# Performance work log

Hardware: AMD Instinct MI355X
Metric: run time of the kernel (lower is better)

The kernel has to match this reference:

```python
import jax, jax.numpy as jnp
import numpy as np

VOCAB = 32000
HID = 1024
LAYERS = 2
BATCH = 16
SEQ = 256


def setup_inputs() -> dict:
    key = jax.random.key(0)
    ks = jax.random.split(key, 8)
    s = 1.0 / np.sqrt(HID)
    x = jax.random.randint(ks[0], (BATCH, SEQ), 0, VOCAB, dtype=jnp.int64)
    embed = jax.random.normal(ks[1], (VOCAB, HID), dtype=jnp.float32) * 0.02
    Wi = jax.random.uniform(ks[2], (LAYERS, HID, HID), jnp.float32, -s, s)
    bi = jax.random.uniform(ks[3], (LAYERS, HID), jnp.float32, -s, s)
    Wh = jax.random.uniform(ks[4], (LAYERS, HID, HID), jnp.float32, -s, s)
    bh = jax.random.uniform(ks[5], (LAYERS, HID), jnp.float32, -s, s)
    Wo = jax.random.uniform(ks[6], (VOCAB, HID), jnp.float32, -s, s)
    bo = jax.random.uniform(ks[7], (VOCAB,), jnp.float32, -s, s)
    return {"x": x, "embed": embed, "Wi": Wi, "bi": bi, "Wh": Wh, "bh": bh, "Wo": Wo, "bo": bo}


def reference(x, embed, Wi, bi, Wh, bh, Wo, bo):
    B, S = x.shape
    L, H, _ = Wi.shape
    emb = embed[x]                      # [B, S, H]
    emb_t = jnp.swapaxes(emb, 0, 1)     # [S, B, H]
    h0 = jnp.zeros((L, B, H), dtype=embed.dtype)

    def step(hidden, x_t):
        inp = x_t
        new_h = []
        for l in range(L):
            inp = jnp.tanh(inp @ Wi[l].T + bi[l] + hidden[l] @ Wh[l].T + bh[l])
            new_h.append(inp)
        hidden = jnp.stack(new_h)       # [L, B, H]
        return hidden, inp              # emit top-layer hidden per step

    hidden, tops = jax.lax.scan(step, h0, emb_t)   # tops: [S, B, H]
    # project all steps at once (same math as per-step fc_out)
    logits = jnp.einsum('sbh,vh->bsv', tops, Wo) + bo  # [B, S, V]
    return logits, hidden
```

## Files before the change

### kernel.cpp

```cpp
#include <hip/hip_runtime.h>
#include <cmath>
#include <cstdint>

#define VOCAB 32000
#define HID   1024
#define BATCH 16
#define SEQ   256
#define NL0   64
#define NL1   128
#define MASTER (NL0 + NL1)
#define NBLK  (NL0 + NL1 + 1)
#define BH    (BATCH * HID)

typedef __attribute__((ext_vector_type(8))) short short8;
typedef __attribute__((ext_vector_type(4))) float f32x4;

__device__ __forceinline__ ushort f2bf(float f) {
  uint u = __builtin_bit_cast(uint, f);
  return (ushort)((u + 0x7FFFu + ((u >> 16) & 1u)) >> 16);
}
__device__ __forceinline__ float bf2f(ushort h) {
  return __builtin_bit_cast(float, (uint)h << 16);
}

#define LOAD8(d, base)                                                        \
  asm volatile(                                                               \
    "global_load_dwordx4 %0, %8, off sc0 sc1\n\t"                             \
    "global_load_dwordx4 %1, %8, off offset:512 sc0 sc1\n\t"                  \
    "global_load_dwordx4 %2, %8, off offset:1024 sc0 sc1\n\t"                 \
    "global_load_dwordx4 %3, %8, off offset:1536 sc0 sc1\n\t"                 \
    "global_load_dwordx4 %4, %8, off offset:2048 sc0 sc1\n\t"                 \
    "global_load_dwordx4 %5, %8, off offset:2560 sc0 sc1\n\t"                 \
    "global_load_dwordx4 %6, %8, off offset:3072 sc0 sc1\n\t"                 \
    "global_load_dwordx4 %7, %8, off offset:3584 sc0 sc1"                     \
    : "=&v"(d[0]), "=&v"(d[1]), "=&v"(d[2]), "=&v"(d[3]),                     \
      "=&v"(d[4]), "=&v"(d[5]), "=&v"(d[6]), "=&v"(d[7])                      \
    : "v"(base) : "memory")

#define WAIT8(d)                                                              \
  asm volatile("s_waitcnt vmcnt(0)"                                           \
    : "+v"(d[0]), "+v"(d[1]), "+v"(d[2]), "+v"(d[3]),                         \
      "+v"(d[4]), "+v"(d[5]), "+v"(d[6]), "+v"(d[7]) :: "memory")

__device__ __forceinline__ void st_coherent(float* p, float v) {
  asm volatile("global_store_dword %0, %1, off sc0 sc1" :: "v"(p), "v"(v) : "memory");
}
__device__ __forceinline__ int ld_rlx(const int* p) {
  return __hip_atomic_load(p, __ATOMIC_RELAXED, __HIP_MEMORY_SCOPE_AGENT);
}
__device__ __forceinline__ void st_rlx(int* p, int v) {
  __hip_atomic_store(p, v, __ATOMIC_RELAXED, __HIP_MEMORY_SCOPE_AGENT);
}

__global__ __launch_bounds__(256) void pre0_gemm(
    const int* __restrict__ x, const float* __restrict__ embed,
    const float* __restrict__ Wi0, const float* __restrict__ bi0,
    const float* __restrict__ bh0, float* __restrict__ pre)
{
  __shared__ float As[32][132];
  __shared__ float Bs[32][132];
  const int tid  = threadIdx.x;
  const int n0   = blockIdx.x * 128;
  const int m0   = blockIdx.y * 128;
  const int lrow = tid >> 3, lkq = tid & 7;
  const int ty   = tid >> 4, tx  = tid & 15;

  const float* arow[4];
#pragma unroll
  for (int q = 0; q < 4; ++q) {
    int m = m0 + lrow + 32 * q;
    int t = m >> 4, b = m & 15;
    arow[q] = embed + (size_t)x[b * SEQ + t] * HID;
  }
  const float* brow = Wi0 + (size_t)(n0 + lrow) * HID;

  float acc[8][8];
#pragma unroll
  for (int i = 0; i < 8; ++i)
#pragma unroll
    for (int j = 0; j < 8; ++j) acc[i][j] = 0.f;

  for (int kt = 0; kt < HID; kt += 32) {
    float4 av[4], bv[4];
#pragma unroll
    for (int q = 0; q < 4; ++q) {
      av[q] = *(const float4*)(arow[q] + kt + lkq * 4);
      bv[q] = *(const float4*)(brow + (size_t)(32 * q) * HID + kt + lkq * 4);
    }
    __syncthreads();
#pragma unroll
    for (int q = 0; q < 4; ++q) {
      int r = lrow + 32 * q;
      As[lkq*4+0][r] = av[q].x; As[lkq*4+1][r] = av[q].y;
      As[lkq*4+2][r] = av[q].z; As[lkq*4+3][r] = av[q].w;
      Bs[lkq*4+0][r] = bv[q].x; Bs[lkq*4+1][r] = bv[q].y;
      Bs[lkq*4+2][r] = bv[q].z; Bs[lkq*4+3][r] = bv[q].w;
    }
    __syncthreads();
#pragma unroll
    for (int kk = 0; kk < 32; ++kk) {
      float4 a0 = *(const float4*)&As[kk][ty * 8];
      float4 a1 = *(const float4*)&As[kk][ty * 8 + 4];
      float4 b0 = *(const float4*)&Bs[kk][tx * 8];
      float4 b1 = *(const float4*)&Bs[kk][tx * 8 + 4];
      float a[8] = {a0.x,a0.y,a0.z,a0.w,a1.x,a1.y,a1.z,a1.w};
      float b[8] = {b0.x,b0.y,b0.z,b0.w,b1.x,b1.y,b1.z,b1.w};
#pragma unroll
      for (int i = 0; i < 8; ++i)
#pragma unroll
        for (int j = 0; j < 8; ++j) acc[i][j] = fmaf(a[i], b[j], acc[i][j]);
    }
  }

#pragma unroll
  for (int i = 0; i < 8; ++i) {
    int m = m0 + ty * 8 + i;
    float* o = pre + (size_t)m * HID + n0 + tx * 8;
#pragma unroll
    for (int j = 0; j < 8; ++j) {
      int n = n0 + tx * 8 + j;
      o[j] = acc[i][j] + bi0[n] + bh0[n];
    }
  }
}

__global__ __launch_bounds__(512) void rnn_scan(
    const float* __restrict__ Wi, const float* __restrict__ Wh,
    const float* __restrict__ bi, const float* __restrict__ bh,
    const float* __restrict__ pre0, float* __restrict__ h0ring,
    float* __restrict__ h1g, float* __restrict__ tops,
    int* __restrict__ bar)
{
  const int tid = threadIdx.x;
  const int blk = blockIdx.x;
  int* go0 = bar + 12 * 32;
  int* go1 = bar + 13 * 32;

  if (blk == MASTER) {
    if (tid == 0) {
      int e0 = 0, e1 = 0;
      while (e0 < SEQ || e1 < SEQ) {
        int s0 = 0, s1 = 0;
#pragma unroll
        for (int i = 0; i < 4; ++i) s0 += ld_rlx(bar + i * 32);
#pragma unroll
        for (int i = 0; i < 8; ++i) s1 += ld_rlx(bar + (4 + i) * 32);
        int n0 = s0 >> 6;
        int n1 = s1 >> 7;
        if (n0 > e0) { e0 = n0; st_rlx(go0, e0); }
        if (n1 > e1) { e1 = n1; st_rlx(go1, e1); }
      }
    }
    return;
  }

  __shared__ float wT[16 * 1024];
  __shared__ float hT[1024 * 16];
  __shared__ float part[2048];
  __shared__ float bias[8];

  const bool isL0 = (blk < NL0);

  if (isL0) {
    const int j = blk;
#pragma unroll
    for (int p = 0; p < 8; ++p) {
      int idx = tid + 512 * p;
      int r = idx >> 8, kq = idx & 255;
      float4 v = *(const float4*)(Wh + ((size_t)(16 * j + r)) * HID + 4 * kq);
      wT[(4*kq+0)*16 + r] = v.x; wT[(4*kq+1)*16 + r] = v.y;
      wT[(4*kq+2)*16 + r] = v.z; wT[(4*kq+3)*16 + r] = v.w;
    }
  } else {
    const int j = blk - NL0;
#pragma unroll
    for (int p = 0; p < 8; ++p) {
      int idx = tid + 512 * p;
      int half = idx >> 11;
      int id2 = idx & 2047;
      int r = id2 >> 8, kq = id2 & 255;
      const float* W = (half ? Wh : Wi) + (size_t)HID * HID;
      float4 v = *(const float4*)(W + ((size_t)(8 * j + r)) * HID + 4 * kq);
      int kb = half * 1024 + 4 * kq;
      wT[(kb+0)*8 + r] = v.x; wT[(kb+1)*8 + r] = v.y;
      wT[(kb+2)*8 + r] = v.z; wT[(kb+3)*8 + r] = v.w;
    }
    if (tid < 8) bias[tid] = bi[HID + 8 * j + tid] + bh[HID + 8 * j + tid];
  }
  __syncthreads();

  const int sb  = tid & 15;
  const int skq = tid >> 4;
  auto hbase = [&](const float* src) {
    return (const float*)((const char*)src + sb * 4096 + skq * 16);
  };
  auto stage_write = [&](const f32x4* d) {
#pragma unroll
    for (int p = 0; p < 8; ++p) {
      int kq = skq + 32 * p;
#pragma unroll
      for (int c = 0; c < 4; ++c) hT[(4*kq+c)*16 + sb] = d[p][c];
    }
  };

  if (isL0) {
    const int bq = tid & 3, rq = (tid >> 2) & 3, ks = tid >> 4;
    for (int u = 0; u < SEQ; ++u) {
      float myPre = 0.f;
      if (tid < 256)
        myPre = pre0[((size_t)u * BATCH + (tid >> 4)) * HID + 16 * blk + (tid & 15)];

      if (tid == 0) {
        while (ld_rlx(go0) < u) __builtin_amdgcn_s_sleep(1);
        const int need = u - 7;
        if (need > 0)
          while (ld_rlx(go1) < need) __builtin_amdgcn_s_sleep(1);
      }
      __syncthreads();

      f32x4 r0[8];
      LOAD8(r0, hbase(h0ring + ((u - 1) & 7) * BH));
      WAIT8(r0);
      stage_write(r0);
      __syncthreads();

      float acc[4][4] = {{0.f}};
#pragma unroll 4
      for (int i = 0; i < 32; ++i) {
        int k = ks + 32 * i;
        float4 hv = *(const float4*)&hT[k * 16 + 4 * bq];
        float4 wv = *(const float4*)&wT[k * 16 + 4 * rq];
        float hb[4] = {hv.x, hv.y, hv.z, hv.w};
        float wr[4] = {wv.x, wv.y, wv.z, wv.w};
#pragma unroll
        for (int b_ = 0; b_ < 4; ++b_)
#pragma unroll
          for (int rj = 0; rj < 4; ++rj)
            acc[b_][rj] = fmaf(hb[b_], wr[rj], acc[b_][rj]);
      }
#pragma unroll
      for (int b_ = 0; b_ < 4; ++b_)
#pragma unroll
        for (int rj = 0; rj < 4; ++rj) {
          float v = acc[b_][rj];
          v += __shfl_xor(v, 16); v += __shfl_xor(v, 32);
          acc[b_][rj] = v;
        }
      const int w = tid >> 6;
      if ((tid & 63) < 16) {
#pragma unroll
        for (int b_ = 0; b_ < 4; ++b_)
#pragma unroll
          for (int rj = 0; rj < 4; ++rj)
            part[w * 256 + (4*bq + b_) * 16 + 4*rq + rj] = acc[b_][rj];
      }
      __syncthreads();
      if (tid < 256) {
        int b = tid >> 4, r = tid & 15;
        float s = myPre;
#pragma unroll
        for (int w2 = 0; w2 < 8; ++w2) s += part[w2 * 256 + b * 16 + r];
        st_coherent(h0ring + (u & 7) * BH + (size_t)b * HID + 16 * blk + r, tanhf(s));
      }
      asm volatile("s_waitcnt vmcnt(0)" ::: "memory");
      __syncthreads();
      if (tid == 0)
        __hip_atomic_fetch_add(bar + (blk & 3) * 32, 1,
                               __ATOMIC_RELAXED, __HIP_MEMORY_SCOPE_AGENT);
    }
  } else {
    const int bq = tid & 3, rq = (tid >> 2) & 1, ks = tid >> 3;
    for (int t = 0; t < SEQ; ++t) {
      if (tid == 0)
        while (ld_rlx(go0) < t + 1) __builtin_amdgcn_s_sleep(1);
      __syncthreads();

      f32x4 r0[8];
      LOAD8(r0, hbase(h0ring + (t & 7) * BH));
      WAIT8(r0);
      stage_write(r0);
      __syncthreads();

      float acc[4][4] = {{0.f}};
#pragma unroll 4
      for (int i = 0; i < 16; ++i) {
        int k = ks + 64 * i;
        float4 hv = *(const float4*)&hT[k * 16 + 4 * bq];
        float4 wv = *(const float4*)&wT[k * 8 + 4 * rq];
        float hb[4] = {hv.x, hv.y, hv.z, hv.w};
        float wr[4] = {wv.x, wv.y, wv.z, wv.w};
#pragma unroll
        for (int b_ = 0; b_ < 4; ++b_)
#pragma unroll
          for (int rj = 0; rj < 4; ++rj)
            acc[b_][rj] = fmaf(hb[b_], wr[rj], acc[b_][rj]);
      }

      if (tid == 0 && t)
        while (ld_rlx(go1) < t) __builtin_amdgcn_s_sleep(1);
      __syncthreads();

      f32x4 r1[8];
      LOAD8(r1, hbase(h1g + ((t - 1) & 1) * BH));
      WAIT8(r1);
      stage_write(r1);
      __syncthreads();

#pragma unroll 4
      for (int i = 0; i < 16; ++i) {
        int k = ks + 64 * i;
        float4 hv = *(const float4*)&hT[k * 16 + 4 * bq];
        float4 wv = *(const float4*)&wT[(1024 + k) * 8 + 4 * rq];
        float hb[4] = {hv.x, hv.y, hv.z, hv.w};
        float wr[4] = {wv.x, wv.y, wv.z, wv.w};
#pragma unroll
        for (int b_ = 0; b_ < 4; ++b_)
#pragma unroll
          for (int rj = 0; rj < 4; ++rj)
            acc[b_][rj] = fmaf(hb[b_], wr[rj], acc[b_][rj]);
      }
#pragma unroll
      for (int b_ = 0; b_ < 4; ++b_)
#pragma unroll
        for (int rj = 0; rj < 4; ++rj) {
          float v = acc[b_][rj];
          v += __shfl_xor(v, 8); v += __shfl_xor(v, 16); v += __shfl_xor(v, 32);
          acc[b_][rj] = v;
        }
      const int w = tid >> 6;
      if ((tid & 63) < 8) {
#pragma unroll
        for (int b_ = 0; b_ < 4; ++b_)
#pragma unroll
          for (int rj = 0; rj < 4; ++rj)
            part[w * 128 + (4*bq + b_) * 8 + 4*rq + rj] = acc[b_][rj];
      }
      __syncthreads();
      if (tid < 128) {
        int b = tid >> 3, r = tid & 7;
        float s = bias[r];
#pragma unroll
        for (int w2 = 0; w2 < 8; ++w2) s += part[w2 * 128 + b * 8 + r];
        int R = 8 * (blk - NL0) + r;
        float v = tanhf(s);
        tops[((size_t)t * BATCH + b) * HID + R] = v;
        st_coherent(h1g + (t & 1) * BH + (size_t)b * HID + R, v);
      }
      asm volatile("s_waitcnt vmcnt(0)" ::: "memory");
      __syncthreads();
      if (tid == 0)
        __hip_atomic_fetch_add(bar + (4 + (blk & 7)) * 32, 1,
                               __ATOMIC_RELAXED, __HIP_MEMORY_SCOPE_AGENT);
    }
  }
}

__global__ __launch_bounds__(512, 1) void proj_mfma(
    const float* __restrict__ tops, const float* __restrict__ Wo,
    const float* __restrict__ bo, float* __restrict__ out)
{
  __shared__ ushort Ahi[256 * 64];
  __shared__ ushort Alo[256 * 64];
  __shared__ ushort Bs [256 * 64];
  const int tid  = threadIdx.x;
  const int m0   = blockIdx.x * 256;
  const int n0   = blockIdx.y * 256;
  const int lane = tid & 63, wv = tid >> 6;
  const int wm   = wv & 3, wn = wv >> 2;
  const int bconst = blockIdx.x;

  f32x4 acc[4][8];
#pragma unroll
  for (int i = 0; i < 4; ++i)
#pragma unroll
    for (int j = 0; j < 8; ++j) acc[i][j] = (f32x4)0.f;

  const int sr = tid >> 4;
  const int sk = (tid & 15) * 4;

  for (int kt = 0; kt < HID; kt += 64) {
    __syncthreads();
#pragma unroll
    for (int p = 0; p < 8; ++p) {
      int r = sr + 32 * p;
      float4 v = *(const float4*)(tops + ((size_t)r * BATCH + bconst) * HID + kt + sk);
      float f[4] = {v.x, v.y, v.z, v.w};
      ushort hi[4], lo[4];
#pragma unroll
      for (int c = 0; c < 4; ++c) {
        hi[c] = f2bf(f[c]);
        lo[c] = f2bf(f[c] - bf2f(hi[c]));
      }
      uint off = (uint)(r * 128 + sk * 2) ^ (uint)((r & 7) << 4);
      *(ushort4*)((char*)Ahi + off) = make_ushort4(hi[0], hi[1], hi[2], hi[3]);
      *(ushort4*)((char*)Alo + off) = make_ushort4(lo[0], lo[1], lo[2], lo[3]);
    }
#pragma unroll
    for (int p = 0; p < 8; ++p) {
      int r = sr + 32 * p;
      float4 v = *(const float4*)(Wo + (size_t)(n0 + r) * HID + kt + sk);
      uint off = (uint)(r * 128 + sk * 2) ^ (uint)((r & 7) << 4);
      *(ushort4*)((char*)Bs + off) =
          make_ushort4(f2bf(v.x), f2bf(v.y), f2bf(v.z), f2bf(v.w));
    }
    __syncthreads();

    const int fr = lane & 15, kg = lane >> 4;
#pragma unroll
    for (int kk = 0; kk < 2; ++kk) {
      short8 bf[8], ah[4], al[4];
#pragma unroll
      for (int nf = 0; nf < 8; ++nf) {
        int row = wn * 128 + nf * 16 + fr;
        uint off = (uint)(row * 128 + kk * 64 + kg * 16) ^ (uint)((row & 7) << 4);
        bf[nf] = *(const short8*)((const char*)Bs + off);
      }
#pragma unroll
      for (int mf = 0; mf < 4; ++mf) {
        int row = wm * 64 + mf * 16 + fr;
        uint off = (uint)(row * 128 + kk * 64 + kg * 16) ^ (uint)((row & 7) << 4);
        ah[mf] = *(const short8*)((const char*)Ahi + off);
        al[mf] = *(const short8*)((const char*)Alo + off);
      }
#pragma unroll
      for (int mf = 0; mf < 4; ++mf)
#pragma unroll
        for (int nf = 0; nf < 8; ++nf) {
          acc[mf][nf] = __builtin_amdgcn_mfma_f32_16x16x32_bf16(
              ah[mf], bf[nf], acc[mf][nf], 0, 0, 0);
          acc[mf][nf] = __builtin_amdgcn_mfma_f32_16x16x32_bf16(
              al[mf], bf[nf], acc[mf][nf], 0, 0, 0);
        }
    }
  }

  const int fr = lane & 15, rg = lane >> 4;
#pragma unroll
  for (int mf = 0; mf < 4; ++mf)
#pragma unroll
    for (int nf = 0; nf < 8; ++nf) {
      int n = n0 + wn * 128 + nf * 16 + fr;
      float bb = bo[n];
#pragma unroll
      for (int j = 0; j < 4; ++j) {
        int m = m0 + wm * 64 + mf * 16 + rg * 4 + j;
        out[(size_t)m * VOCAB + n] = acc[mf][nf][j] + bb;
      }
    }
}

__global__ void copy_hidden(const float* __restrict__ h0ring,
                            const float* __restrict__ tops,
                            float* __restrict__ outh)
{
  int i = blockIdx.x * 256 + threadIdx.x;
  int l = i >> 14, rem = i & 16383;
  outh[i] = (l == 0) ? h0ring[7 * BH + rem]
                     : tops[(size_t)(SEQ - 1) * BH + rem];
}

extern "C" void kernel_launch(void* const* d_in, const int* in_sizes, int n_in,
                              void* d_out, int out_size, void* d_ws, size_t ws_size,
                              hipStream_t stream)
{
  const int*   x     = (const int*)d_in[0];
  const float* embed = (const float*)d_in[1];
  const float* Wi    = (const float*)d_in[2];
  const float* bi    = (const float*)d_in[3];
  const float* Wh    = (const float*)d_in[4];
  const float* bh    = (const float*)d_in[5];
  const float* Wo    = (const float*)d_in[6];
  const float* bo    = (const float*)d_in[7];
  float* out = (float*)d_out;

  char* ws = (char*)d_ws;
  float* pre0   = (float*)(ws);
  float* tops   = (float*)(ws + (16u << 20));
  float* h0ring = (float*)(ws + (32u << 20));
  float* h1g    = (float*)(ws + (32u << 20) + 524288);
  int*   bar    = (int*)  (ws + (32u << 20) + 655360);

  hipMemsetAsync(h0ring, 0, 655360 + 4096, stream);

  pre0_gemm<<<dim3(8, 32), dim3(256), 0, stream>>>(x, embed, Wi, bi, bh, pre0);

  void* args[] = { (void*)&Wi, (void*)&Wh, (void*)&bi, (void*)&bh,
                   (void*)&pre0, (void*)&h0ring, (void*)&h1g, (void*)&tops,
                   (void*)&bar };
  hipLaunchCooperativeKernel((void*)rnn_scan, dim3(NBLK), dim3(512), args, 0, stream);

  proj_mfma<<<dim3(16, 125), dim3(512), 0, stream>>>(tops, Wo, bo, out);

  copy_hidden<<<dim3(128), dim3(256), 0, stream>>>(
      h0ring, tops, out + (size_t)BATCH * SEQ * VOCAB);
}
```

Before: 2.895 ms.

## Fuse output projection into persistent RNN scan kernel with ticketed tiles

Folds the vocabulary projection GEMM into the cooperative scan kernel. Idle extra blocks (192..255) and the scan blocks, once their recurrence finishes, grab 256x256 output tiles from an atomic ticket counter. Each tile waits until the layer-1 step counter covers its rows, so the projection of early timesteps overlaps the remaining recurrence. The M tiles are now time-major and the output row is remapped on store. Tops stores become coherent so the in-kernel readers see them. The trade-off is a larger shared-memory pool per block and possible contention between projection blocks and the latency-critical scan blocks.

```diff
diff --git a/kernel.cpp b/kernel.cpp
--- a/kernel.cpp
+++ b/kernel.cpp
@@ -8,9 +8,12 @@
 #define SEQ   256
 #define NL0   64
 #define NL1   128
-#define MASTER (NL0 + NL1)
-#define NBLK  (NL0 + NL1 + 1)
+#define MASTER 192
+#define NBLK  256
 #define BH    (BATCH * HID)
+#define NTILE_M 16
+#define NTILE_N 125
+#define NTILES  (NTILE_M * NTILE_N)
 
 typedef __attribute__((ext_vector_type(8))) short short8;
 typedef __attribute__((ext_vector_type(4))) float f32x4;
@@ -129,15 +132,121 @@
     const float* __restrict__ bi, const float* __restrict__ bh,
     const float* __restrict__ pre0, float* __restrict__ h0ring,
     float* __restrict__ h1g, float* __restrict__ tops,
-    int* __restrict__ bar)
+    const float* __restrict__ Wo, const float* __restrict__ bo,
+    float* __restrict__ out, int* __restrict__ bar)
 {
+  __shared__ __align__(16) char pool[139328];
+  __shared__ int tkt_s;
   const int tid = threadIdx.x;
   const int blk = blockIdx.x;
-  int* go0 = bar + 12 * 32;
-  int* go1 = bar + 13 * 32;
-
-  if (blk == MASTER) {
-    if (tid == 0) {
+  int* go0    = bar + 12 * 32;
+  int* go1    = bar + 13 * 32;
+  int* ticket = bar + 14 * 32;
+
+  auto proj_tiles = [&]() {
+    ushort* Ahi = (ushort*)pool;
+    ushort* Alo = Ahi + 16384;
+    ushort* Bs  = Alo + 16384;
+    const int lane = tid & 63, wv = tid >> 6;
+    const int wm = wv & 3, wn = wv >> 2;
+    const int sr = tid >> 4;
+    const int sk = (tid & 15) * 4;
+    for (;;) {
+      if (tid == 0)
+        tkt_s = __hip_atomic_fetch_add(ticket, 1, __ATOMIC_RELAXED,
+                                       __HIP_MEMORY_SCOPE_AGENT);
+      __syncthreads();
+      const int T = tkt_s;
+      if (T >= NTILES) break;
+      const int mt = T / NTILE_N, nt = T % NTILE_N;
+      if (tid == 0) {
+        int need = 16 * (mt + 1); if (need > SEQ) need = SEQ;
+        while (ld_rlx(go1) < need) __builtin_amdgcn_s_sleep(2);
+      }
+      __syncthreads();
+      const int m0 = mt * 256, n0 = nt * 256;
+
+      f32x4 acc[4][8];
+#pragma unroll
+      for (int i = 0; i < 4; ++i)
+#pragma unroll
+        for (int j = 0; j < 8; ++j) acc[i][j] = (f32x4)0.f;
+
+      for (int kt = 0; kt < HID; kt += 64) {
+        __syncthreads();
+#pragma unroll
+        for (int p = 0; p < 8; ++p) {
+          int r = sr + 32 * p;
+          float4 v = *(const float4*)(tops + (size_t)(m0 + r) * HID + kt + sk);
+          float f[4] = {v.x, v.y, v.z, v.w};
+          ushort hi[4], lo[4];
+#pragma unroll
+          for (int c = 0; c < 4; ++c) {
+            hi[c] = f2bf(f[c]);
+            lo[c] = f2bf(f[c] - bf2f(hi[c]));
+          }
+          uint off = (uint)(r * 128 + sk * 2) ^ (uint)((r & 7) << 4);
+          *(ushort4*)((char*)Ahi + off) = make_ushort4(hi[0], hi[1], hi[2], hi[3]);
+          *(ushort4*)((char*)Alo + off) = make_ushort4(lo[0], lo[1], lo[2], lo[3]);
+        }
+#pragma unroll
+        for (int p = 0; p < 8; ++p) {
+          int r = sr + 32 * p;
+          float4 v = *(const float4*)(Wo + (size_t)(n0 + r) * HID + kt + sk);
+          uint off = (uint)(r * 128 + sk * 2) ^ (uint)((r & 7) << 4);
+          *(ushort4*)((char*)Bs + off) =
+              make_ushort4(f2bf(v.x), f2bf(v.y), f2bf(v.z), f2bf(v.w));
+        }
+        __syncthreads();
+
+        const int fr = lane & 15, kg = lane >> 4;
+#pragma unroll
+        for (int kk = 0; kk < 2; ++kk) {
+          short8 bf[8], ah[4], al[4];
+#pragma unroll
+          for (int nf = 0; nf < 8; ++nf) {
+            int row = wn * 128 + nf * 16 + fr;
+            uint off = (uint)(row * 128 + kk * 64 + kg * 16) ^ (uint)((row & 7) << 4);
+            bf[nf] = *(const short8*)((const char*)Bs + off);
+          }
+#pragma unroll
+          for (int mf = 0; mf < 4; ++mf) {
+            int row = wm * 64 + mf * 16 + fr;
+            uint off = (uint)(row * 128 + kk * 64 + kg * 16) ^ (uint)((row & 7) << 4);
+            ah[mf] = *(const short8*)((const char*)Ahi + off);
+            al[mf] = *(const short8*)((const char*)Alo + off);
+          }
+#pragma unroll
+          for (int mf = 0; mf < 4; ++mf)
+#pragma unroll
+            for (int nf = 0; nf < 8; ++nf) {
+              acc[mf][nf] = __builtin_amdgcn_mfma_f32_16x16x32_bf16(
+                  ah[mf], bf[nf], acc[mf][nf], 0, 0, 0);
+              acc[mf][nf] = __builtin_amdgcn_mfma_f32_16x16x32_bf16(
+                  al[mf], bf[nf], acc[mf][nf], 0, 0, 0);
+            }
+        }
+      }
+
+      const int fr = lane & 15, rg = lane >> 4;
+#pragma unroll
+      for (int mf = 0; mf < 4; ++mf)
+#pragma unroll
+        for (int nf = 0; nf < 8; ++nf) {
+          int n = n0 + wn * 128 + nf * 16 + fr;
+          float bb = bo[n];
+#pragma unroll
+          for (int j = 0; j < 4; ++j) {
+            int m = m0 + wm * 64 + mf * 16 + rg * 4 + j;
+            int orow = (m & 15) * 256 + (m >> 4);
+            out[(size_t)orow * VOCAB + n] = acc[mf][nf][j] + bb;
+          }
+        }
+    }
+  };
+
+  if (blk >= MASTER) {
+    if (blk == MASTER && tid == 0) {
       int e0 = 0, e1 = 0;
       while (e0 < SEQ || e1 < SEQ) {
         int s0 = 0, s1 = 0;
@@ -151,13 +260,14 @@
         if (n1 > e1) { e1 = n1; st_rlx(go1, e1); }
       }
     }
+    proj_tiles();
     return;
   }
 
-  __shared__ float wT[16 * 1024];
-  __shared__ float hT[1024 * 16];
-  __shared__ float part[2048];
-  __shared__ float bias[8];
+  float* wT   = (float*)pool;
+  float* hT   = wT + 16384;
+  float* part = hT + 16384;
+  float* bias = part + 2048;
 
   const bool isL0 = (blk < NL0);
 
@@ -343,7 +453,7 @@
         for (int w2 = 0; w2 < 8; ++w2) s += part[w2 * 128 + b * 8 + r];
         int R = 8 * (blk - NL0) + r;
         float v = tanhf(s);
-        tops[((size_t)t * BATCH + b) * HID + R] = v;
+        st_coherent(&tops[((size_t)t * BATCH + b) * HID + R], v);
         st_coherent(h1g + (t & 1) * BH + (size_t)b * HID + R, v);
       }
       asm volatile("s_waitcnt vmcnt(0)" ::: "memory");
@@ -353,100 +463,9 @@
                                __ATOMIC_RELAXED, __HIP_MEMORY_SCOPE_AGENT);
     }
   }
-}
-
-__global__ __launch_bounds__(512, 1) void proj_mfma(
-    const float* __restrict__ tops, const float* __restrict__ Wo,
-    const float* __restrict__ bo, float* __restrict__ out)
-{
-  __shared__ ushort Ahi[256 * 64];
-  __shared__ ushort Alo[256 * 64];
-  __shared__ ushort Bs [256 * 64];
-  const int tid  = threadIdx.x;
-  const int m0   = blockIdx.x * 256;
-  const int n0   = blockIdx.y * 256;
-  const int lane = tid & 63, wv = tid >> 6;
-  const int wm   = wv & 3, wn = wv >> 2;
-  const int bconst = blockIdx.x;
-
-  f32x4 acc[4][8];
-#pragma unroll
-  for (int i = 0; i < 4; ++i)
-#pragma unroll
-    for (int j = 0; j < 8; ++j) acc[i][j] = (f32x4)0.f;
-
-  const int sr = tid >> 4;
-  const int sk = (tid & 15) * 4;
-
-  for (int kt = 0; kt < HID; kt += 64) {
-    __syncthreads();
-#pragma unroll
-    for (int p = 0; p < 8; ++p) {
-      int r = sr + 32 * p;
-      float4 v = *(const float4*)(tops + ((size_t)r * BATCH + bconst) * HID + kt + sk);
-      float f[4] = {v.x, v.y, v.z, v.w};
-      ushort hi[4], lo[4];
-#pragma unroll
-      for (int c = 0; c < 4; ++c) {
-        hi[c] = f2bf(f[c]);
-        lo[c] = f2bf(f[c] - bf2f(hi[c]));
-      }
-      uint off = (uint)(r * 128 + sk * 2) ^ (uint)((r & 7) << 4);
-      *(ushort4*)((char*)Ahi + off) = make_ushort4(hi[0], hi[1], hi[2], hi[3]);
-      *(ushort4*)((char*)Alo + off) = make_ushort4(lo[0], lo[1], lo[2], lo[3]);
-    }
-#pragma unroll
-    for (int p = 0; p < 8; ++p) {
-      int r = sr + 32 * p;
-      float4 v = *(const float4*)(Wo + (size_t)(n0 + r) * HID + kt + sk);
-      uint off = (uint)(r * 128 + sk * 2) ^ (uint)((r & 7) << 4);
-      *(ushort4*)((char*)Bs + off) =
-          make_ushort4(f2bf(v.x), f2bf(v.y), f2bf(v.z), f2bf(v.w));
-    }
-    __syncthreads();
-
-    const int fr = lane & 15, kg = lane >> 4;
-#pragma unroll
-    for (int kk = 0; kk < 2; ++kk) {
-      short8 bf[8], ah[4], al[4];
-#pragma unroll
-      for (int nf = 0; nf < 8; ++nf) {
-        int row = wn * 128 + nf * 16 + fr;
-        uint off = (uint)(row * 128 + kk * 64 + kg * 16) ^ (uint)((row & 7) << 4);
-        bf[nf] = *(const short8*)((const char*)Bs + off);
-      }
-#pragma unroll
-      for (int mf = 0; mf < 4; ++mf) {
-        int row = wm * 64 + mf * 16 + fr;
-        uint off = (uint)(row * 128 + kk * 64 + kg * 16) ^ (uint)((row & 7) << 4);
-        ah[mf] = *(const short8*)((const char*)Ahi + off);
-        al[mf] = *(const short8*)((const char*)Alo + off);
-      }
-#pragma unroll
-      for (int mf = 0; mf < 4; ++mf)
-#pragma unroll
-        for (int nf = 0; nf < 8; ++nf) {
-          acc[mf][nf] = __builtin_amdgcn_mfma_f32_16x16x32_bf16(
-              ah[mf], bf[nf], acc[mf][nf], 0, 0, 0);
-          acc[mf][nf] = __builtin_amdgcn_mfma_f32_16x16x32_bf16(
-              al[mf], bf[nf], acc[mf][nf], 0, 0, 0);
-        }
-    }
-  }
-
-  const int fr = lane & 15, rg = lane >> 4;
-#pragma unroll
-  for (int mf = 0; mf < 4; ++mf)
-#pragma unroll
-    for (int nf = 0; nf < 8; ++nf) {
-      int n = n0 + wn * 128 + nf * 16 + fr;
-      float bb = bo[n];
-#pragma unroll
-      for (int j = 0; j < 4; ++j) {
-        int m = m0 + wm * 64 + mf * 16 + rg * 4 + j;
-        out[(size_t)m * VOCAB + n] = acc[mf][nf][j] + bb;
-      }
-    }
+
+  __syncthreads();
+  proj_tiles();
 }
 
 __global__ void copy_hidden(const float* __restrict__ h0ring,
@@ -486,10 +505,8 @@
 
   void* args[] = { (void*)&Wi, (void*)&Wh, (void*)&bi, (void*)&bh,
                    (void*)&pre0, (void*)&h0ring, (void*)&h1g, (void*)&tops,
-                   (void*)&bar };
+                   (void*)&Wo, (void*)&bo, (void*)&out, (void*)&bar };
   hipLaunchCooperativeKernel((void*)rnn_scan, dim3(NBLK), dim3(512), args, 0, stream);
-
-  proj_mfma<<<dim3(16, 125), dim3(512), 0, stream>>>(tops, Wo, bo, out);
 
   copy_hidden<<<dim3(128), dim3(256), 0, stream>>>(
       h0ring, tops, out + (size_t)BATCH * SEQ * VOCAB);
```

After: 2.801 ms. -3.2%, faster.
